# Kernel tuning notes

Measured on AMD Instinct MI355X. Metric: run time of the kernel, lower is better.

The kernel has to match this reference:

```python
import jax, jax.numpy as jnp
import numpy as np
import math

B, N, D, K = 4, 255, 256, 128
NODE_FEATURES_OFFSET = 128
MAX_Z = 101
NUM_EDGES = 2 * NODE_FEATURES_OFFSET + 1  # 257
NUM_DIR_KERNEL = 128  # FourierDirectionalEmbed num_kernel
ECFG_F = 20  # synthetic electron-config feature dim


def setup_inputs() -> dict:
    key = jax.random.key(0)
    ks = jax.random.split(key, 16)
    positions = jax.random.normal(ks[0], (B, N, 3), dtype=jnp.float32) * 3.0
    atomic_numbers = jax.random.randint(ks[1], (B, N), 1, MAX_Z, dtype=jnp.int32)
    s = 0.02
    emb_z = jax.random.normal(ks[2], (MAX_Z + 1, D), dtype=jnp.float32) * s
    electron_config = jax.random.uniform(ks[3], (MAX_Z + 1, ECFG_F), dtype=jnp.float32)
    config_W = jax.random.normal(ks[4], (ECFG_F, D), dtype=jnp.float32) * s
    config_b = jnp.zeros((D,), dtype=jnp.float32)
    mult_W = jax.random.normal(ks[5], (NODE_FEATURES_OFFSET, D), dtype=jnp.float32) * s
    charge_W = jax.random.normal(ks[6], (NODE_FEATURES_OFFSET, D), dtype=jnp.float32) * s
    gbf_means = jax.random.uniform(ks[7], (K,), dtype=jnp.float32, minval=0.0, maxval=7.0)
    gbf_stds = jax.random.uniform(ks[8], (K,), dtype=jnp.float32, minval=0.0, maxval=3.0)
    gbf_mul = jax.random.normal(ks[9], (NUM_EDGES,), dtype=jnp.float32).at[0].set(0.0)  # padding_idx=0
    gbf_bias = (jax.random.normal(ks[10], (NUM_EDGES,), dtype=jnp.float32) * 0.1).at[0].set(0.0)
    proj1_W = jax.random.normal(ks[11], (K, K), dtype=jnp.float32) * (1.0 / math.sqrt(K))
    proj1_b = jnp.zeros((K,), dtype=jnp.float32)
    proj2_W = jax.random.normal(ks[12], (K, D), dtype=jnp.float32) * (1.0 / math.sqrt(K))
    proj2_b = jnp.zeros((D,), dtype=jnp.float32)
    dir_W = jax.random.normal(ks[13], (2 * NUM_DIR_KERNEL, D), dtype=jnp.float32) * (1.0 / math.sqrt(2 * NUM_DIR_KERNEL))
    dir_b = jnp.zeros((D,), dtype=jnp.float32)
    return dict(positions=positions, atomic_numbers=atomic_numbers, emb_z=emb_z,
                electron_config=electron_config, config_W=config_W, config_b=config_b,
                mult_W=mult_W, charge_W=charge_W, gbf_means=gbf_means, gbf_stds=gbf_stds,
                gbf_mul=gbf_mul, gbf_bias=gbf_bias, proj1_W=proj1_W, proj1_b=proj1_b,
                proj2_W=proj2_W, proj2_b=proj2_b, dir_W=dir_W, dir_b=dir_b)


def _angular_freqs():
    min_angle = 1e-4
    half = NUM_DIR_KERNEL // 2
    wl_az = jnp.exp(jnp.linspace(math.log(2 * min_angle), math.log(2 * 2 * math.pi), half))
    wl_po = jnp.exp(jnp.linspace(math.log(2 * min_angle), math.log(2 * math.pi), half))
    return (2 * math.pi / wl_az).astype(jnp.float32), (2 * math.pi / wl_po).astype(jnp.float32)


def _forward(positions, atomic_numbers, emb_z, electron_config, config_W, config_b,
             mult_W, charge_W, gbf_means, gbf_stds, gbf_mul, gbf_bias,
             proj1_W, proj1_b, proj2_W, proj2_b, dir_W, dir_b):
    b = positions.shape[0]
    # add graph-level (CLS) token: zero position, z = MAX_Z = 101
    pos = jnp.concatenate([jnp.zeros_like(positions[:, :1]), positions], axis=1)  # [B,Np,3]
    z = jnp.concatenate([jnp.full_like(atomic_numbers[:, :1], MAX_Z), atomic_numbers], axis=1)  # [B,Np]
    npad = pos.shape[1]

    # --- node embedding: nuclear + electronic + multiplicity(1) + charge(0) ---
    elec = electron_config[z] @ config_W + config_b            # [B,Np,D]
    elec = elec.at[:, 0, :].set(0.0)                            # cls_token row zeroed
    node = emb_z[z] + elec + mult_W[1] + charge_W[0]           # [B,Np,D]

    # --- pairwise geometry: directions[b,i,j] = pos[j] - pos[i] ---
    d = pos[:, None, :, :] - pos[:, :, None, :]                # [B,Np,Np,3]
    sq = jnp.sum(d * d, axis=-1)
    dist = jnp.sqrt(sq + 1e-12)                                # [B,Np,Np]
    nd = d / (dist[..., None] + 1e-5)                          # normed directions, eps per source
    eye = jnp.eye(npad, dtype=bool)[None, :, :]
    x_safe = jnp.where(eye, 1.0, nd[..., 0])
    y_safe = jnp.where(eye, 0.0, nd[..., 1])
    azimuth = jnp.arctan2(y_safe, x_safe)                      # [B,Np,Np]
    polar = jnp.arccos(jnp.clip(nd[..., 2], -1.0 + 1e-6, 1.0 - 1e-6))

    # --- FourierDirectionalEmbed ---
    f_az, f_po = _angular_freqs()
    ph_az = azimuth[..., None] * f_az                          # [B,Np,Np,64]
    ph_po = polar[..., None] * f_po
    sinusoids = jnp.concatenate([jnp.sin(ph_az), jnp.cos(ph_az),
                                 jnp.sin(ph_po), jnp.cos(ph_po)], axis=-1)  # [B,Np,Np,256]
    dir_out = sinusoids @ dir_W + dir_b                        # [B,Np,Np,D]

    # --- Gaussian3DEmbed ---
    zi = z[:, :, None]
    zj = z[:, None, :] + NODE_FEATURES_OFFSET
    mul = gbf_mul[zi] + gbf_mul[zj]                            # sum over the 2 edge-type entries
    bias = gbf_bias[zi] + gbf_bias[zj]                         # [B,Np,Np]
    gx = (mul * dist + bias)[..., None]                        # [B,Np,Np,1] -> broadcast to K
    std = jnp.abs(gbf_stds) + 0.01
    pi_c = 3.14159
    gauss = jnp.exp(-0.5 * ((gx - gbf_means) / std) ** 2) / ((2 * pi_c) ** 0.5 * std)  # [B,Np,Np,K]
    h = jax.nn.gelu(gauss @ proj1_W + proj1_b, approximate=False)
    gbf_out = h @ proj2_W + proj2_b                            # [B,Np,Np,D]

    return node, gbf_out, dir_out


def reference(positions, atomic_numbers, emb_z, electron_config, config_W, config_b,
              mult_W, charge_W, gbf_means, gbf_stds, gbf_mul, gbf_bias,
              proj1_W, proj1_b, proj2_W, proj2_b, dir_W, dir_b):
    return _forward(positions, atomic_numbers, emb_z, electron_config, config_W, config_b,
                    mult_W, charge_W, gbf_means, gbf_stds, gbf_mul, gbf_bias,
                    proj1_W, proj1_b, proj2_W, proj2_b, dir_W, dir_b)
```

## Files before the change

### kernel.cpp

```cpp
#include <hip/hip_runtime.h>
#include <math.h>

typedef __bf16 bf16x8 __attribute__((ext_vector_type(8)));
typedef __bf16 bf16x4 __attribute__((ext_vector_type(4)));
typedef float f32x4 __attribute__((ext_vector_type(4)));

#define PI_D 3.14159265358979323846

__global__ void prep_kernel(const float* __restrict__ dir_W,
                            const float* __restrict__ proj1_W,
                            const float* __restrict__ proj2_W,
                            const float* __restrict__ gbf_stds,
                            __bf16* __restrict__ dirP, __bf16* __restrict__ p1P,
                            __bf16* __restrict__ p2P,
                            float* __restrict__ f_az, float* __restrict__ f_po,
                            float* __restrict__ inv_std, float* __restrict__ coef) {
  int tid = threadIdx.x + blockIdx.x * blockDim.x;
  int nth = gridDim.x * blockDim.x;
  for (int o = tid; o < 256 * 256; o += nth) {
    int j = o & 7, l = (o >> 3) & 63, ks = (o >> 9) & 7, nt = o >> 12;
    int d = nt * 16 + (l & 15);
    int s = ks * 32 + (l >> 4) * 8 + j;
    dirP[o] = (__bf16)dir_W[s * 256 + d];
  }
  for (int o = tid; o < 128 * 128; o += nth) {
    int j = o & 7, l = (o >> 3) & 63, ks = (o >> 9) & 3, nt = o >> 11;
    int ko = nt * 16 + (l & 15);
    int ki = ks * 32 + (l >> 4) * 8 + j;
    p1P[o] = (__bf16)proj1_W[ki * 128 + ko];
  }
  for (int o = tid; o < 128 * 256; o += nth) {
    int j = o & 7, l = (o >> 3) & 63, ks = (o >> 9) & 3, nt = o >> 11;
    int d = nt * 16 + (l & 15);
    int k = ks * 32 + (l >> 4) * 8 + j;
    p2P[o] = (__bf16)proj2_W[k * 256 + d];
  }
  if (blockIdx.x == 0 && threadIdx.x < 64) {
    int q = threadIdx.x;
    double l0 = log(2.0 * 1e-4);
    double l1a = log(2.0 * 2.0 * PI_D);
    double l1p = log(2.0 * PI_D);
    double ta = l0 + (l1a - l0) * (double)q / 63.0;
    double tp = l0 + (l1p - l0) * (double)q / 63.0;
    f_az[q] = (float)(2.0 * PI_D / exp(ta));
    f_po[q] = (float)(2.0 * PI_D / exp(tp));
  }
  if (blockIdx.x == 1 && threadIdx.x < 128) {
    int k = threadIdx.x;
    float sd = fabsf(gbf_stds[k]) + 0.01f;
    inv_std[k] = 1.0f / sd;
    coef[k] = (float)(1.0 / (sqrt(2.0 * 3.14159) * (double)sd));
  }
}

__global__ void node_kernel(const int* __restrict__ an, const float* __restrict__ emb_z,
                            const float* __restrict__ ec, const float* __restrict__ cW,
                            const float* __restrict__ cb, const float* __restrict__ mult_W,
                            const float* __restrict__ charge_W, float* __restrict__ out_node) {
  int bi = blockIdx.x;
  int b = bi >> 8, i = bi & 255;
  int d = threadIdx.x;
  int z = (i == 0) ? 101 : an[b * 255 + i - 1];
  float elec = 0.0f;
  if (i != 0) {
    for (int f = 0; f < 20; ++f) elec += ec[z * 20 + f] * cW[f * 256 + d];
    elec += cb[d];
  }
  float v = emb_z[z * 256 + d] + elec + mult_W[256 + d] + charge_W[d];
  __builtin_nontemporal_store(v, &out_node[(size_t)bi * 256 + d]);
}

__global__ __launch_bounds__(256, 4) void pair_kernel(
    const float* __restrict__ positions, const int* __restrict__ atomic_numbers,
    const float* __restrict__ gbf_means, const float* __restrict__ gbf_mul,
    const float* __restrict__ gbf_bias, const float* __restrict__ proj1_b,
    const float* __restrict__ proj2_b, const float* __restrict__ dir_b,
    const __bf16* __restrict__ dirP, const __bf16* __restrict__ p1P,
    const __bf16* __restrict__ p2P, const float* __restrict__ f_az,
    const float* __restrict__ f_po, const float* __restrict__ inv_stdv,
    const float* __restrict__ coefv, float* __restrict__ out_gbf,
    float* __restrict__ out_dir) {
  __shared__ __align__(16) __bf16 buf[64 * 136];
  __shared__ float s_az[64], s_po[64], s_gx[64];

  const int tid = threadIdx.x;
  const int bid = blockIdx.x;
  const int jt = bid & 3;
  const int i = (bid >> 2) & 255;
  const int b = bid >> 10;
  const int j0 = jt * 64;
  const long pairbase = ((long)(b * 256 + i)) * 256 + j0;

  const int lane = tid & 63, wv = tid >> 6;
  const int lr = lane & 15, kb = lane >> 4;

  if (tid < 64) {
    int p = tid, j = j0 + p;
    float pxi = 0.f, pyi = 0.f, pzi = 0.f, pxj = 0.f, pyj = 0.f, pzj = 0.f;
    if (i != 0) { const float* q = positions + ((size_t)b * 255 + (i - 1)) * 3; pxi = q[0]; pyi = q[1]; pzi = q[2]; }
    if (j != 0) { const float* q = positions + ((size_t)b * 255 + (j - 1)) * 3; pxj = q[0]; pyj = q[1]; pzj = q[2]; }
    float dx = pxj - pxi, dy = pyj - pyi, dz = pzj - pzi;
    float sq = dx * dx + dy * dy + dz * dz;
    float dist = sqrtf(sq + 1e-12f);
    float inv = 1.0f / (dist + 1e-5f);
    float ndx = dx * inv, ndy = dy * inv, ndz = dz * inv;
    bool diag = (i == j);
    float xs = diag ? 1.0f : ndx;
    float ys = diag ? 0.0f : ndy;
    s_az[p] = atan2f(ys, xs);
    float cz = fminf(fmaxf(ndz, -1.0f + 1e-6f), 1.0f - 1e-6f);
    s_po[p] = acosf(cz);
    int zi = (i == 0) ? 101 : atomic_numbers[b * 255 + i - 1];
    int zj = ((j == 0) ? 101 : atomic_numbers[b * 255 + j - 1]) + 128;
    float mul = gbf_mul[zi] + gbf_mul[zj];
    float bia = gbf_bias[zi] + gbf_bias[zj];
    s_gx[p] = mul * dist + bia;
  }
  __syncthreads();

  f32x4 acc[4][4];
#pragma unroll
  for (int mtl = 0; mtl < 4; ++mtl)
#pragma unroll
    for (int np = 0; np < 4; ++np) acc[mtl][np] = (f32x4){0.f, 0.f, 0.f, 0.f};

  for (int half = 0; half < 2; ++half) {
#pragma unroll
    for (int it = 0; it < 2; ++it) {
      int job = tid + it * 256;
      int p = job >> 3, g = job & 7;
      int q0 = g * 8;
      float ang = half ? s_po[p] : s_az[p];
      const float* ft = half ? f_po : f_az;
      bf16x8 sv, cv;
#pragma unroll
      for (int t = 0; t < 8; ++t) {
        float ph = ang * ft[q0 + t];
        double r = (double)ph * 0.15915494309189535;
        double fr = r - rint(r);
        float frf = (float)fr;
        sv[t] = (__bf16)__builtin_amdgcn_sinf(frf);
        cv[t] = (__bf16)__builtin_amdgcn_cosf(frf);
      }
      *(bf16x8*)(buf + p * 136 + q0) = sv;
      *(bf16x8*)(buf + p * 136 + 64 + q0) = cv;
    }
    __syncthreads();
#pragma unroll
    for (int ksl = 0; ksl < 4; ++ksl) {
      int ks = half * 4 + ksl;
      bf16x8 bfr[4];
#pragma unroll
      for (int np = 0; np < 4; ++np)
        bfr[np] = *(const bf16x8*)(buf + (np * 16 + lr) * 136 + ksl * 32 + kb * 8);
#pragma unroll
      for (int mtl = 0; mtl < 4; ++mtl) {
        int mtile = mtl * 4 + wv;
        bf16x8 af = *(const bf16x8*)(dirP + (((size_t)mtile * 8 + ks) * 64 + lane) * 8);
#pragma unroll
        for (int np = 0; np < 4; ++np)
          acc[mtl][np] = __builtin_amdgcn_mfma_f32_16x16x32_bf16(af, bfr[np], acc[mtl][np], 0, 0, 0);
      }
    }
    __syncthreads();
  }

#pragma unroll
  for (int mtl = 0; mtl < 4; ++mtl) {
    int dcol0 = (mtl * 4 + wv) * 16 + kb * 4;
    f32x4 bias = *(const f32x4*)(dir_b + dcol0);
#pragma unroll
    for (int np = 0; np < 4; ++np) {
      f32x4 v = acc[mtl][np] + bias;
      __builtin_nontemporal_store(v, (f32x4*)(out_dir + (pairbase + np * 16 + lr) * 256 + dcol0));
    }
  }

#pragma unroll
  for (int it = 0; it < 4; ++it) {
    int job = tid + it * 256;
    int p = job >> 4, g = job & 15;
    int k0 = g * 8;
    float gx = s_gx[p];
    bf16x8 gv;
#pragma unroll
    for (int t = 0; t < 8; ++t) {
      int k = k0 + t;
      float x = (gx - gbf_means[k]) * inv_stdv[k];
      gv[t] = (__bf16)(exp2f(-0.72134752044448170f * x * x) * coefv[k]);
    }
    *(bf16x8*)(buf + p * 136 + k0) = gv;
  }
  __syncthreads();

  f32x4 acc1[2][4];
#pragma unroll
  for (int mtl = 0; mtl < 2; ++mtl)
#pragma unroll
    for (int np = 0; np < 4; ++np) acc1[mtl][np] = (f32x4){0.f, 0.f, 0.f, 0.f};
#pragma unroll
  for (int ksl = 0; ksl < 4; ++ksl) {
    bf16x8 bfr[4];
#pragma unroll
    for (int np = 0; np < 4; ++np)
      bfr[np] = *(const bf16x8*)(buf + (np * 16 + lr) * 136 + ksl * 32 + kb * 8);
#pragma unroll
    for (int mtl = 0; mtl < 2; ++mtl) {
      int mtile = mtl * 4 + wv;
      bf16x8 af = *(const bf16x8*)(p1P + (((size_t)mtile * 4 + ksl) * 64 + lane) * 8);
#pragma unroll
      for (int np = 0; np < 4; ++np)
        acc1[mtl][np] = __builtin_amdgcn_mfma_f32_16x16x32_bf16(af, bfr[np], acc1[mtl][np], 0, 0, 0);
    }
  }
  __syncthreads();

#pragma unroll
  for (int mtl = 0; mtl < 2; ++mtl) {
    int ko0 = (mtl * 4 + wv) * 16 + kb * 4;
    f32x4 pb = *(const f32x4*)(proj1_b + ko0);
#pragma unroll
    for (int np = 0; np < 4; ++np) {
      f32x4 hv = acc1[mtl][np] + pb;
      bf16x4 hb;
#pragma unroll
      for (int r = 0; r < 4; ++r) {
        float v = hv[r];
        v = 0.5f * v * (1.0f + erff(v * 0.70710678118654752f));
        hb[r] = (__bf16)v;
      }
      *(bf16x4*)(buf + (np * 16 + lr) * 136 + ko0) = hb;
    }
  }
  __syncthreads();

  f32x4 acc2[4][4];
#pragma unroll
  for (int mtl = 0; mtl < 4; ++mtl)
#pragma unroll
    for (int np = 0; np < 4; ++np) acc2[mtl][np] = (f32x4){0.f, 0.f, 0.f, 0.f};
#pragma unroll
  for (int ksl = 0; ksl < 4; ++ksl) {
    bf16x8 bfr[4];
#pragma unroll
    for (int np = 0; np < 4; ++np)
      bfr[np] = *(const bf16x8*)(buf + (np * 16 + lr) * 136 + ksl * 32 + kb * 8);
#pragma unroll
    for (int mtl = 0; mtl < 4; ++mtl) {
      int mtile = mtl * 4 + wv;
      bf16x8 af = *(const bf16x8*)(p2P + (((size_t)mtile * 4 + ksl) * 64 + lane) * 8);
#pragma unroll
      for (int np = 0; np < 4; ++np)
        acc2[mtl][np] = __builtin_amdgcn_mfma_f32_16x16x32_bf16(af, bfr[np], acc2[mtl][np], 0, 0, 0);
    }
  }
#pragma unroll
  for (int mtl = 0; mtl < 4; ++mtl) {
    int dcol0 = (mtl * 4 + wv) * 16 + kb * 4;
    f32x4 bias = *(const f32x4*)(proj2_b + dcol0);
#pragma unroll
    for (int np = 0; np < 4; ++np) {
      f32x4 v = acc2[mtl][np] + bias;
      __builtin_nontemporal_store(v, (f32x4*)(out_gbf + (pairbase + np * 16 + lr) * 256 + dcol0));
    }
  }
}

extern "C" void kernel_launch(void* const* d_in, const int* in_sizes, int n_in,
                              void* d_out, int out_size, void* d_ws, size_t ws_size,
                              hipStream_t stream) {
  const float* positions = (const float*)d_in[0];
  const int* atomic_numbers = (const int*)d_in[1];
  const float* emb_z = (const float*)d_in[2];
  const float* electron_config = (const float*)d_in[3];
  const float* config_W = (const float*)d_in[4];
  const float* config_b = (const float*)d_in[5];
  const float* mult_W = (const float*)d_in[6];
  const float* charge_W = (const float*)d_in[7];
  const float* gbf_means = (const float*)d_in[8];
  const float* gbf_stds = (const float*)d_in[9];
  const float* gbf_mul = (const float*)d_in[10];
  const float* gbf_bias = (const float*)d_in[11];
  const float* proj1_W = (const float*)d_in[12];
  const float* proj1_b = (const float*)d_in[13];
  const float* proj2_W = (const float*)d_in[14];
  const float* proj2_b = (const float*)d_in[15];
  const float* dir_W = (const float*)d_in[16];
  const float* dir_b = (const float*)d_in[17];

  float* out = (float*)d_out;
  float* out_node = out;
  float* out_gbf = out + 262144;
  float* out_dir = out + 262144 + 67108864;

  char* ws = (char*)d_ws;
  __bf16* dirP = (__bf16*)(ws);
  __bf16* p1P = (__bf16*)(ws + 131072);
  __bf16* p2P = (__bf16*)(ws + 131072 + 32768);
  float* f_az = (float*)(ws + 229376);
  float* f_po = (float*)(ws + 229376 + 256);
  float* inv_std = (float*)(ws + 229376 + 512);
  float* coef = (float*)(ws + 229376 + 1024);

  prep_kernel<<<64, 256, 0, stream>>>(dir_W, proj1_W, proj2_W, gbf_stds, dirP, p1P,
                                      p2P, f_az, f_po, inv_std, coef);
  node_kernel<<<1024, 256, 0, stream>>>(atomic_numbers, emb_z, electron_config,
                                        config_W, config_b, mult_W, charge_W, out_node);
  pair_kernel<<<4096, 256, 0, stream>>>(positions, atomic_numbers, gbf_means, gbf_mul,
                                        gbf_bias, proj1_b, proj2_b, dir_b, dirP, p1P,
                                        p2P, f_az, f_po, inv_std, coef, out_gbf, out_dir);
}
```

Measured before the change: 160.7 us.

## Reorder pair kernel stages, double-buffer LDS, and use lightweight barriers

Reorders the pair kernel so the Gaussian MLP branch runs first and the directional Fourier branch runs after it. LDS is split into two buffers so the GELU output and the directional sin/cos features can be written without an extra barrier, and the directional GEMM now does all eight k-steps in one pass over both buffers. __syncthreads is replaced by a custom barrier that waits only on LDS counters, not global memory, so outstanding nontemporal stores no longer block progress. Frequency tables are hoisted into registers. The cost is roughly double the LDS per block (about 35 KB), which may reduce occupancy.

```diff
diff --git a/kernel.cpp b/kernel.cpp
--- a/kernel.cpp
+++ b/kernel.cpp
@@ -6,6 +6,13 @@
 typedef float f32x4 __attribute__((ext_vector_type(4)));
 
 #define PI_D 3.14159265358979323846
+
+__device__ __forceinline__ void bar_lds() {
+  __builtin_amdgcn_sched_barrier(0);
+  asm volatile("s_waitcnt lgkmcnt(0)" ::: "memory");
+  __builtin_amdgcn_s_barrier();
+  __builtin_amdgcn_sched_barrier(0);
+}
 
 __global__ void prep_kernel(const float* __restrict__ dir_W,
                             const float* __restrict__ proj1_W,
@@ -80,7 +87,8 @@
     const float* __restrict__ f_po, const float* __restrict__ inv_stdv,
     const float* __restrict__ coefv, float* __restrict__ out_gbf,
     float* __restrict__ out_dir) {
-  __shared__ __align__(16) __bf16 buf[64 * 136];
+  __shared__ __align__(16) __bf16 bufA[64 * 136];
+  __shared__ __align__(16) __bf16 bufB[64 * 136];
   __shared__ float s_az[64], s_po[64], s_gx[64];
 
   const int tid = threadIdx.x;
@@ -93,6 +101,19 @@
 
   const int lane = tid & 63, wv = tid >> 6;
   const int lr = lane & 15, kb = lane >> 4;
+
+  const int g = tid & 15;
+  const bool az = g < 8;
+  const int q0 = (g & 7) * 8;
+  const int k0g = g * 8;
+  const int prow = tid >> 4;
+
+  float ftv[8];
+  {
+    const float* ft = az ? f_az : f_po;
+#pragma unroll
+    for (int t = 0; t < 8; ++t) ftv[t] = ft[q0 + t];
+  }
 
   if (tid < 64) {
     int p = tid, j = j0 + p;
@@ -116,82 +137,22 @@
     float bia = gbf_bias[zi] + gbf_bias[zj];
     s_gx[p] = mul * dist + bia;
   }
-  __syncthreads();
-
-  f32x4 acc[4][4];
-#pragma unroll
-  for (int mtl = 0; mtl < 4; ++mtl)
-#pragma unroll
-    for (int np = 0; np < 4; ++np) acc[mtl][np] = (f32x4){0.f, 0.f, 0.f, 0.f};
-
-  for (int half = 0; half < 2; ++half) {
-#pragma unroll
-    for (int it = 0; it < 2; ++it) {
-      int job = tid + it * 256;
-      int p = job >> 3, g = job & 7;
-      int q0 = g * 8;
-      float ang = half ? s_po[p] : s_az[p];
-      const float* ft = half ? f_po : f_az;
-      bf16x8 sv, cv;
-#pragma unroll
-      for (int t = 0; t < 8; ++t) {
-        float ph = ang * ft[q0 + t];
-        double r = (double)ph * 0.15915494309189535;
-        double fr = r - rint(r);
-        float frf = (float)fr;
-        sv[t] = (__bf16)__builtin_amdgcn_sinf(frf);
-        cv[t] = (__bf16)__builtin_amdgcn_cosf(frf);
-      }
-      *(bf16x8*)(buf + p * 136 + q0) = sv;
-      *(bf16x8*)(buf + p * 136 + 64 + q0) = cv;
-    }
-    __syncthreads();
-#pragma unroll
-    for (int ksl = 0; ksl < 4; ++ksl) {
-      int ks = half * 4 + ksl;
-      bf16x8 bfr[4];
-#pragma unroll
-      for (int np = 0; np < 4; ++np)
-        bfr[np] = *(const bf16x8*)(buf + (np * 16 + lr) * 136 + ksl * 32 + kb * 8);
-#pragma unroll
-      for (int mtl = 0; mtl < 4; ++mtl) {
-        int mtile = mtl * 4 + wv;
-        bf16x8 af = *(const bf16x8*)(dirP + (((size_t)mtile * 8 + ks) * 64 + lane) * 8);
-#pragma unroll
-        for (int np = 0; np < 4; ++np)
-          acc[mtl][np] = __builtin_amdgcn_mfma_f32_16x16x32_bf16(af, bfr[np], acc[mtl][np], 0, 0, 0);
-      }
-    }
-    __syncthreads();
-  }
-
-#pragma unroll
-  for (int mtl = 0; mtl < 4; ++mtl) {
-    int dcol0 = (mtl * 4 + wv) * 16 + kb * 4;
-    f32x4 bias = *(const f32x4*)(dir_b + dcol0);
-#pragma unroll
-    for (int np = 0; np < 4; ++np) {
-      f32x4 v = acc[mtl][np] + bias;
-      __builtin_nontemporal_store(v, (f32x4*)(out_dir + (pairbase + np * 16 + lr) * 256 + dcol0));
-    }
-  }
+  bar_lds();
 
 #pragma unroll
   for (int it = 0; it < 4; ++it) {
-    int job = tid + it * 256;
-    int p = job >> 4, g = job & 15;
-    int k0 = g * 8;
+    int p = prow + it * 16;
     float gx = s_gx[p];
     bf16x8 gv;
 #pragma unroll
     for (int t = 0; t < 8; ++t) {
-      int k = k0 + t;
+      int k = k0g + t;
       float x = (gx - gbf_means[k]) * inv_stdv[k];
       gv[t] = (__bf16)(exp2f(-0.72134752044448170f * x * x) * coefv[k]);
     }
-    *(bf16x8*)(buf + p * 136 + k0) = gv;
-  }
-  __syncthreads();
+    *(bf16x8*)(bufA + p * 136 + k0g) = gv;
+  }
+  bar_lds();
 
   f32x4 acc1[2][4];
 #pragma unroll
@@ -203,7 +164,7 @@
     bf16x8 bfr[4];
 #pragma unroll
     for (int np = 0; np < 4; ++np)
-      bfr[np] = *(const bf16x8*)(buf + (np * 16 + lr) * 136 + ksl * 32 + kb * 8);
+      bfr[np] = *(const bf16x8*)(bufA + (np * 16 + lr) * 136 + ksl * 32 + kb * 8);
 #pragma unroll
     for (int mtl = 0; mtl < 2; ++mtl) {
       int mtile = mtl * 4 + wv;
@@ -213,7 +174,6 @@
         acc1[mtl][np] = __builtin_amdgcn_mfma_f32_16x16x32_bf16(af, bfr[np], acc1[mtl][np], 0, 0, 0);
     }
   }
-  __syncthreads();
 
 #pragma unroll
   for (int mtl = 0; mtl < 2; ++mtl) {
@@ -229,10 +189,10 @@
         v = 0.5f * v * (1.0f + erff(v * 0.70710678118654752f));
         hb[r] = (__bf16)v;
       }
-      *(bf16x4*)(buf + (np * 16 + lr) * 136 + ko0) = hb;
-    }
-  }
-  __syncthreads();
+      *(bf16x4*)(bufB + (np * 16 + lr) * 136 + ko0) = hb;
+    }
+  }
+  bar_lds();
 
   f32x4 acc2[4][4];
 #pragma unroll
@@ -244,7 +204,7 @@
     bf16x8 bfr[4];
 #pragma unroll
     for (int np = 0; np < 4; ++np)
-      bfr[np] = *(const bf16x8*)(buf + (np * 16 + lr) * 136 + ksl * 32 + kb * 8);
+      bfr[np] = *(const bf16x8*)(bufB + (np * 16 + lr) * 136 + ksl * 32 + kb * 8);
 #pragma unroll
     for (int mtl = 0; mtl < 4; ++mtl) {
       int mtile = mtl * 4 + wv;
@@ -262,6 +222,60 @@
     for (int np = 0; np < 4; ++np) {
       f32x4 v = acc2[mtl][np] + bias;
       __builtin_nontemporal_store(v, (f32x4*)(out_gbf + (pairbase + np * 16 + lr) * 256 + dcol0));
+    }
+  }
+  bar_lds();
+
+#pragma unroll
+  for (int it = 0; it < 4; ++it) {
+    int p = prow + it * 16;
+    float ang = az ? s_az[p] : s_po[p];
+    bf16x8 sv, cv;
+#pragma unroll
+    for (int t = 0; t < 8; ++t) {
+      float ph = ang * ftv[t];
+      double r = (double)ph * 0.15915494309189535;
+      double fr = r - rint(r);
+      float frf = (float)fr;
+      sv[t] = (__bf16)__builtin_amdgcn_sinf(frf);
+      cv[t] = (__bf16)__builtin_amdgcn_cosf(frf);
+    }
+    __bf16* base = (az ? bufA : bufB) + p * 136 + q0;
+    *(bf16x8*)(base) = sv;
+    *(bf16x8*)(base + 64) = cv;
+  }
+  bar_lds();
+
+  f32x4 acc[4][4];
+#pragma unroll
+  for (int mtl = 0; mtl < 4; ++mtl)
+#pragma unroll
+    for (int np = 0; np < 4; ++np) acc[mtl][np] = (f32x4){0.f, 0.f, 0.f, 0.f};
+#pragma unroll
+  for (int ks = 0; ks < 8; ++ks) {
+    const __bf16* sbuf = (ks < 4) ? bufA : bufB;
+    int ksl = ks & 3;
+    bf16x8 bfr[4];
+#pragma unroll
+    for (int np = 0; np < 4; ++np)
+      bfr[np] = *(const bf16x8*)(sbuf + (np * 16 + lr) * 136 + ksl * 32 + kb * 8);
+#pragma unroll
+    for (int mtl = 0; mtl < 4; ++mtl) {
+      int mtile = mtl * 4 + wv;
+      bf16x8 af = *(const bf16x8*)(dirP + (((size_t)mtile * 8 + ks) * 64 + lane) * 8);
+#pragma unroll
+      for (int np = 0; np < 4; ++np)
+        acc[mtl][np] = __builtin_amdgcn_mfma_f32_16x16x32_bf16(af, bfr[np], acc[mtl][np], 0, 0, 0);
+    }
+  }
+#pragma unroll
+  for (int mtl = 0; mtl < 4; ++mtl) {
+    int dcol0 = (mtl * 4 + wv) * 16 + kb * 4;
+    f32x4 bias = *(const f32x4*)(dir_b + dcol0);
+#pragma unroll
+    for (int np = 0; np < 4; ++np) {
+      f32x4 v = acc[mtl][np] + bias;
+      __builtin_nontemporal_store(v, (f32x4*)(out_dir + (pairbase + np * 16 + lr) * 256 + dcol0));
     }
   }
 }
```

New measurement: 164.6 us. 2.4% more time.
